# Optimization experiments

Hardware: AMD Instinct MI355X
Metric: run time of the kernel (lower is better)

Reference implementation:

```python
import jax, jax.numpy as jnp
import numpy as np

T, B, EMBED, HEADS = 1024, 32, 512, 8
HEAD = EMBED // HEADS      # per-head value size (= head_dim = 64)
KEYD = 16                  # key_size hard-coded to 16 in MultiheadAttention
MEM_SLOTS, TOPK = 8, 3
NUM_GATES = 2 * EMBED      # gate_style='unit' -> 2*mem_size


def layer_norm(x, g, b, eps=1e-5):
    mu = jnp.mean(x, axis=-1, keepdims=True)
    var = jnp.var(x, axis=-1, keepdims=True)
    return (x - mu) * jax.lax.rsqrt(var + eps) * g + b


def mha(q_src, kv_src, Wq, bq, Wk, bk, Wv, bv, use_topk):
    # q from q_src (RelationalMemory passes 'memory' arg as query source),
    # k/v from kv_src ('input' arg). No 1/sqrt(d) scaling in original code.
    Bq, Sq = q_src.shape[0], q_src.shape[1]
    Sk = kv_src.shape[1]
    q = (q_src @ Wq + bq).reshape(Bq, Sq, HEADS, KEYD)
    k = (kv_src @ Wk + bk).reshape(Bq, Sk, HEADS, KEYD)
    v = (kv_src @ Wv + bv).reshape(Bq, Sk, HEADS, HEAD)
    probs = jax.nn.softmax(jnp.einsum('bqhd,bkhd->bhqk', q, k), axis=-1)
    if use_topk:
        _, idx = jax.lax.top_k(probs, TOPK)  # (B,H,Sq,TOPK)
        mask = jnp.sum(jax.nn.one_hot(idx, Sk, dtype=probs.dtype), axis=-2)
        probs = probs * mask  # post-softmax top-k gate (scatter of ones)
    out = jnp.einsum('bhqk,bkhd->bqhd', probs, v)
    return out.reshape(Bq, Sq, EMBED)


def setup_inputs() -> dict:
    rng = jax.random.key(0)
    ks = jax.random.split(rng, 12)

    def n(k, shape, s=0.02):
        return jax.random.normal(k, shape, dtype=jnp.float32) * s

    # initial_state: eye(mem_slots) zero-padded to mem_size, per batch element
    mem0 = jnp.pad(jnp.eye(MEM_SLOTS, dtype=jnp.float32), ((0, 0), (0, EMBED - MEM_SLOTS)))
    return {
        'query': jax.random.normal(ks[0], (T, B, EMBED), jnp.float32),
        'key': jax.random.normal(ks[1], (T, B, EMBED), jnp.float32),
        'memory': jnp.tile(mem0[None], (B, 1, 1)),
        'W_in': n(ks[2], (EMBED, EMBED)), 'b_in': jnp.zeros((EMBED,), jnp.float32),
        'Wq': n(ks[3], (EMBED, KEYD * HEADS)), 'bq': jnp.zeros((KEYD * HEADS,), jnp.float32),
        'Wk': n(ks[4], (EMBED, KEYD * HEADS)), 'bk': jnp.zeros((KEYD * HEADS,), jnp.float32),
        'Wv': n(ks[5], (EMBED, EMBED)), 'bv': jnp.zeros((EMBED,), jnp.float32),
        'W_mlp': n(ks[6], (EMBED, EMBED)), 'b_mlp': jnp.zeros((EMBED,), jnp.float32),
        'g1': jnp.ones((EMBED,), jnp.float32), 'be1': jnp.zeros((EMBED,), jnp.float32),
        'g2': jnp.ones((EMBED,), jnp.float32), 'be2': jnp.zeros((EMBED,), jnp.float32),
        'w_rep': jax.random.normal(ks[7], (EMBED,), jnp.float32),
        'W_ig': n(ks[8], (EMBED, NUM_GATES)), 'b_ig': jnp.zeros((NUM_GATES,), jnp.float32),
        'W_mg': n(ks[9], (MEM_SLOTS, EMBED, NUM_GATES)), 'b_mg': jnp.zeros((MEM_SLOTS, NUM_GATES), jnp.float32),
        'forget_bias': jnp.asarray(1.0, jnp.float32),
        'input_bias': jnp.asarray(0.0, jnp.float32),
    }


def reference(query, key, memory, W_in, b_in, Wq, bq, Wk, bk, Wv, bv,
              W_mlp, b_mlp, g1, be1, g2, be2, w_rep, W_ig, b_ig,
              W_mg, b_mg, forget_bias, input_bias):
    # query only shape-checked by the torch module; key carries the content
    inputs = jnp.transpose(key, (1, 0, 2))          # (B, T, E)
    x = inputs @ W_in + b_in                        # input_projector
    # attend_over_memory (num_blocks=1): memory slots query the tokens, top-k write
    attended = mha(memory, x, Wq, bq, Wk, bk, Wv, bv, use_topk=True)
    m = layer_norm(memory + attended, g1, be1)
    mlp = jax.nn.relu(m @ W_mlp + b_mlp)            # attention_mlp_layers=1
    new_mem = layer_norm(m + mlp, g2, be2)
    # gating (gate_style='unit')
    gi = jnp.mean(jax.nn.relu(w_rep * x), axis=1) @ W_ig + b_ig      # RepeatLinear -> (B, 2E)
    gm = jnp.einsum('bsm,smn->bsn', jnp.tanh(memory), W_mg) + b_mg   # GroupLinearLayer -> (B, S, 2E)
    in_g, f_g = jnp.split(gi[:, None, :] + gm, 2, axis=-1)
    in_g = jax.nn.sigmoid(in_g + input_bias)
    f_g = jax.nn.sigmoid(f_g + forget_bias)
    new_mem = in_g * jnp.tanh(new_mem) + f_g * memory
    # broadcast read: every token queries the updated memory (no top-k)
    hx = mha(x, new_mem, Wq, bq, Wk, bk, Wv, bv, use_topk=False)     # (B, T, E)
    return jnp.transpose(hx, (1, 0, 2))             # (T, B, E) as in torch forward
```

## Files before the change

### kernel.cpp

```cpp
#include <hip/hip_runtime.h>
#include <stdint.h>

typedef unsigned short u16;
typedef __bf16 bf16x8 __attribute__((ext_vector_type(8)));
typedef float f32x4 __attribute__((ext_vector_type(4)));


__device__ __forceinline__ u16 f2b(float f) {
  union { __bf16 h; u16 u; } v; v.h = (__bf16)f; return v.u;
}
__device__ __forceinline__ float b2f(u16 h) {
  union { uint32_t u; float f; } v; v.u = ((uint32_t)h) << 16; return v.f;
}
__device__ __forceinline__ void gload_lds16(const void* g, void* l) {
  __builtin_amdgcn_global_load_lds(
      (const __attribute__((address_space(1))) unsigned int*)g,
      (__attribute__((address_space(3))) unsigned int*)l, 16, 0, 0);
}

__global__ void k_prep(const float* __restrict__ W_in, u16* __restrict__ WxT,
                       const float* __restrict__ Wv, u16* __restrict__ WvT,
                       const float* __restrict__ mem, float* __restrict__ tm,
                       const float* __restrict__ b_in, float* __restrict__ bfull,
                       const float* __restrict__ Wk, const float* __restrict__ Wq,
                       u16* __restrict__ WkqTr, u16* __restrict__ WinB,
                       const float* __restrict__ W_mlp, u16* __restrict__ WmlpT,
                       const float* __restrict__ key, u16* __restrict__ keyB) {
  int idx = blockIdx.x * 256 + threadIdx.x;
  if (idx < 262144) {
    int k = idx >> 9, n = idx & 511;
    WxT[n * 512 + k] = f2b(W_in[idx]);
  } else if (idx < 524288) {
    int j = idx - 262144;
    int k = j >> 9, n = j & 511;
    WvT[n * 512 + k] = f2b(Wv[j]);
  } else if (idx < 655360) {
    int j = idx - 524288;
    tm[j] = tanhf(mem[j]);
  } else if (idx < 655872) {
    int j = idx - 655360;
    bfull[j] = b_in[j];
  } else if (idx < 786944) {
    int i = idx - 655872;
    int j = i >> 9, n = i & 511;
    WkqTr[i] = f2b(j < 128 ? Wk[n * 128 + j] : Wq[n * 128 + j - 128]);
  } else if (idx < 1049088) {
    int i = idx - 786944;
    WinB[i] = f2b(W_in[i]);
  } else if (idx < 1311232) {
    int i = idx - 1049088;
    int k = i >> 9, n = i & 511;
    WmlpT[n * 512 + k] = f2b(W_mlp[i]);
  } else {
    int i = idx - 1311232;
    int r = i >> 6, e8 = i & 63;
    int b = r >> 10, t = r & 1023;
    const float* src = key + ((size_t)(t * 32 + b) << 9) + e8 * 8;
    float4 lo = *(const float4*)src;
    float4 hi = *(const float4*)(src + 4);
    bf16x8 o;
    o[0] = (__bf16)lo.x; o[1] = (__bf16)lo.y; o[2] = (__bf16)lo.z; o[3] = (__bf16)lo.w;
    o[4] = (__bf16)hi.x; o[5] = (__bf16)hi.y; o[6] = (__bf16)hi.z; o[7] = (__bf16)hi.w;
    *(bf16x8*)(keyB + ((size_t)r << 9) + e8 * 8) = o;
  }
}

__global__ __launch_bounds__(256) void k_wprep2(
    const u16* __restrict__ A, const u16* __restrict__ Bt, u16* __restrict__ WxT,
    const float* __restrict__ b_in, const float* __restrict__ Wk, const float* __restrict__ Wq,
    const float* __restrict__ bk, const float* __restrict__ bq, float* __restrict__ bfull,
    const float* __restrict__ memory, const float* __restrict__ bqf, float* __restrict__ qm)
{
  const int bid = blockIdx.x;
  const int tid = threadIdx.x;
  if (bid < 8) {
    __shared__ u16 As[128 * 32];
    __shared__ u16 Bs[128 * 32];
    const int m0 = (bid & 1) * 128;
    const int n0 = (bid >> 1) * 128;
    const int lane = tid & 63;
    const int wid = tid >> 6;
    const int wm = (wid >> 1) * 64;
    const int wn = (wid & 1) * 64;
    f32x4 acc[4][4];
    #pragma unroll
    for (int i = 0; i < 4; ++i)
      #pragma unroll
      for (int j = 0; j < 4; ++j) acc[i][j] = (f32x4){0.f, 0.f, 0.f, 0.f};
    for (int kt = 0; kt < 16; ++kt) {
      const int k0 = kt << 5;
      __syncthreads();
      #pragma unroll
      for (int c = 0; c < 2; ++c) {
        int o = c * 2048 + tid * 8;
        int row = o >> 5, ck = o & 31;
        gload_lds16(A + (size_t)(m0 + row) * 512 + k0 + ck, As + o);
        gload_lds16(Bt + (size_t)(n0 + row) * 512 + k0 + ck, Bs + o);
      }
      __syncthreads();
      const int r = lane & 15;
      const int kb = (lane >> 4) * 8;
      bf16x8 af[4], bfr[4];
      #pragma unroll
      for (int i = 0; i < 4; ++i) {
        af[i]  = *(const bf16x8*)(As + (wm + i * 16 + r) * 32 + kb);
        bfr[i] = *(const bf16x8*)(Bs + (wn + i * 16 + r) * 32 + kb);
      }
      #pragma unroll
      for (int i = 0; i < 4; ++i)
        #pragma unroll
        for (int j = 0; j < 4; ++j)
          acc[i][j] = __builtin_amdgcn_mfma_f32_16x16x32_bf16(af[i], bfr[j], acc[i][j], 0, 0, 0);
    }
    const int cl = lane & 15;
    const int rl = (lane >> 4) * 4;
    #pragma unroll
    for (int j = 0; j < 4; ++j) {
      const int col = n0 + wn + j * 16 + cl;
      #pragma unroll
      for (int i = 0; i < 4; ++i) {
        #pragma unroll
        for (int rr = 0; rr < 4; ++rr) {
          const int row = m0 + wm + i * 16 + rl + rr;
          WxT[(size_t)(512 + row) * 512 + col] = f2b(acc[i][j][rr]);
        }
      }
    }
  } else if (bid == 8) {
    __shared__ float bs[512];
    const int j = tid;
    bs[tid] = b_in[tid];
    bs[256 + tid] = b_in[256 + tid];
    __syncthreads();
    const float* W = (j < 128) ? (Wk + j) : (Wq + j - 128);
    float a = 0.f;
    #pragma unroll 8
    for (int n = 0; n < 512; ++n)
      a += bs[n] * W[(size_t)n * 128];
    bfull[512 + j] = a + ((j < 128) ? bk[j] : bq[j - 128]);
  } else {
    const int bs_ = bid - 9;
    const int b = bs_ >> 3, s = bs_ & 7;
    const int col = tid & 127, half = tid >> 7;
    __shared__ float mrow[512];
    __shared__ float part[2][128];
    *(float2*)&mrow[tid * 2] = *(const float2*)&memory[(size_t)(b * 8 + s) * 512 + tid * 2];
    __syncthreads();
    float a = 0.f;
    const int e0 = half * 256;
    for (int e = 0; e < 256; ++e)
      a += mrow[e0 + e] * Wq[(size_t)(e0 + e) * 128 + col];
    part[half][col] = a;
    __syncthreads();
    if (tid < 128)
      qm[(size_t)(b * 8 + s) * 128 + tid] = part[0][tid] + part[1][tid] + bqf[tid];
  }
}

__global__ __launch_bounds__(256) void gemm_xkq(
    const u16* __restrict__ keyB, const u16* __restrict__ Bt,
    const float* __restrict__ bias, u16* __restrict__ x, u16* __restrict__ kq)
{
  __shared__ u16 smem[16384];
  u16* As = smem;
  u16* Bs = smem + 8192;
  const int tid = threadIdx.x;
  const int bid = blockIdx.x;
  const int wgid = (bid & 7) * 192 + (bid >> 3);
  const int m0 = (wgid / 6) * 128;
  const int n0 = (wgid % 6) * 128;
  const int lane = tid & 63;
  const int wid = tid >> 6;
  const int wm = (wid >> 1) * 64;
  const int wn = (wid & 1) * 64;

  f32x4 acc[4][4];
  #pragma unroll
  for (int i = 0; i < 4; ++i)
    #pragma unroll
    for (int j = 0; j < 4; ++j) acc[i][j] = (f32x4){0.f, 0.f, 0.f, 0.f};

  for (int kt = 0; kt < 8; ++kt) {
    const int k0 = kt << 6;
    __syncthreads();
    #pragma unroll
    for (int c = 0; c < 4; ++c) {
      const int q = c * 256 + tid;
      const int row = q >> 3;
      const int c8 = q & 7;
      const int lc = c8 ^ (row & 7);
      gload_lds16(keyB + (size_t)(m0 + row) * 512 + k0 + lc * 8, As + q * 8);
      gload_lds16(Bt   + (size_t)(n0 + row) * 512 + k0 + lc * 8, Bs + q * 8);
    }
    __syncthreads();
    const int r = lane & 15;
    const int hi = lane >> 4;
    bf16x8 af[4][2], bfr[4][2];
    #pragma unroll
    for (int i = 0; i < 4; ++i) {
      const int ra = wm + i * 16 + r;
      const int rb = wn + i * 16 + r;
      #pragma unroll
      for (int kk = 0; kk < 2; ++kk) {
        af[i][kk]  = *(const bf16x8*)(As + ra * 64 + (((kk * 4 + hi)) ^ (ra & 7)) * 8);
        bfr[i][kk] = *(const bf16x8*)(Bs + rb * 64 + (((kk * 4 + hi)) ^ (rb & 7)) * 8);
      }
    }
    #pragma unroll
    for (int kk = 0; kk < 2; ++kk)
      #pragma unroll
      for (int i = 0; i < 4; ++i)
        #pragma unroll
        for (int j = 0; j < 4; ++j)
          acc[i][j] = __builtin_amdgcn_mfma_f32_16x16x32_bf16(af[i][kk], bfr[j][kk], acc[i][j], 0, 0, 0);
  }
  __syncthreads();
  u16* Cs = smem;
  const int cl = lane & 15;
  const int rl = (lane >> 4) * 4;
  #pragma unroll
  for (int j = 0; j < 4; ++j) {
    const int lcol = wn + j * 16 + cl;
    const float bsv = bias[n0 + lcol];
    #pragma unroll
    for (int i = 0; i < 4; ++i)
      #pragma unroll
      for (int rr = 0; rr < 4; ++rr)
        Cs[(wm + i * 16 + rl + rr) * 128 + lcol] = f2b(acc[i][j][rr] + bsv);
  }
  __syncthreads();
  #pragma unroll
  for (int c = 0; c < 8; ++c) {
    const int chunk = c * 256 + tid;
    const int row = chunk >> 4, c8 = chunk & 15;
    uint4 v = *(const uint4*)&Cs[row * 128 + c8 * 8];
    if (n0 < 512)
      *(uint4*)(x + (size_t)(m0 + row) * 512 + n0 + c8 * 8) = v;
    else
      *(uint4*)(kq + (size_t)(m0 + row) * 256 + (n0 - 512) + c8 * 8) = v;
  }
}

__global__ __launch_bounds__(256) void k_scores_topk(
    const float* __restrict__ qm, const u16* __restrict__ kq,
    const u16* __restrict__ x, float* __restrict__ p3, u16* __restrict__ XW)
{
  const int b = blockIdx.x, h = blockIdx.y, s = blockIdx.z;
  const int tid = threadIdx.x;
  __shared__ float swv[4];
  __shared__ int   swi[4];
  __shared__ float ssv[4];

  float q[16];
  const float* qp = qm + ((size_t)(b * 8 + s) * 128 + h * 16);
  #pragma unroll
  for (int d = 0; d < 16; ++d) q[d] = qp[d];

  float sc[4];
  #pragma unroll
  for (int j = 0; j < 4; ++j) {
    const int t = j * 256 + tid;
    const u16* kr = kq + ((size_t)(b * 1024 + t)) * 256 + h * 16;
    uint4 v0 = *(const uint4*)kr;
    uint4 v1 = *(const uint4*)(kr + 8);
    const u16* p0 = (const u16*)&v0;
    const u16* p1 = (const u16*)&v1;
    float a = 0.f;
    #pragma unroll
    for (int d = 0; d < 8; ++d) a += q[d] * b2f(p0[d]);
    #pragma unroll
    for (int d = 0; d < 8; ++d) a += q[8 + d] * b2f(p1[d]);
    sc[j] = a;
  }

  int   seli[3];
  float selv[3];
  float ssum = 0.f;
  #pragma unroll
  for (int pass = 0; pass < 3; ++pass) {
    float bv_ = -1e30f; int bi_ = 1 << 30;
    #pragma unroll
    for (int j = 0; j < 4; ++j) {
      const int t = j * 256 + tid;
      bool skip = false;
      for (int k = 0; k < pass; ++k) skip |= (t == seli[k]);
      float v = skip ? -1e30f : sc[j];
      if (v > bv_ || (v == bv_ && t < bi_)) { bv_ = v; bi_ = t; }
    }
    #pragma unroll
    for (int o = 32; o > 0; o >>= 1) {
      float ov = __shfl_xor(bv_, o);
      int   oi = __shfl_xor(bi_, o);
      if (ov > bv_ || (ov == bv_ && oi < bi_)) { bv_ = ov; bi_ = oi; }
    }
    __syncthreads();
    if ((tid & 63) == 0) { swv[tid >> 6] = bv_; swi[tid >> 6] = bi_; }
    __syncthreads();
    float wv = swv[0]; int wi = swi[0];
    #pragma unroll
    for (int w = 1; w < 4; ++w) {
      float ov = swv[w]; int oi = swi[w];
      if (ov > wv || (ov == wv && oi < wi)) { wv = ov; wi = oi; }
    }
    selv[pass] = wv; seli[pass] = wi;

    if (pass == 0) {
      float se = 0.f;
      #pragma unroll
      for (int j = 0; j < 4; ++j) se += __expf(sc[j] - wv);
      #pragma unroll
      for (int o = 32; o > 0; o >>= 1) se += __shfl_xor(se, o);
      __syncthreads();
      if ((tid & 63) == 0) ssv[tid >> 6] = se;
      __syncthreads();
      ssum = ssv[0] + ssv[1] + ssv[2] + ssv[3];
    }
  }

  const float m0v = selv[0];
  const float inv = 1.f / ssum;
  const float p0 = __expf(selv[0] - m0v) * inv;
  const float p1 = __expf(selv[1] - m0v) * inv;
  const float p2 = __expf(selv[2] - m0v) * inv;
  if (tid == 0) {
    const size_t base = (size_t)(b * 64 + h * 8 + s);
    p3[base * 4 + 0] = p0;
    p3[base * 4 + 1] = p1;
    p3[base * 4 + 2] = p2;
    p3[base * 4 + 3] = p0 + p1 + p2;
  }
  if (tid < 64) {
    const u16* xb = x + ((size_t)b << 19) + tid * 8;
    uint4 a0 = *(const uint4*)(xb + ((size_t)seli[0] << 9));
    uint4 a1 = *(const uint4*)(xb + ((size_t)seli[1] << 9));
    uint4 a2 = *(const uint4*)(xb + ((size_t)seli[2] << 9));
    const u16* e0 = (const u16*)&a0;
    const u16* e1 = (const u16*)&a1;
    const u16* e2 = (const u16*)&a2;
    u16 ov[8];
    #pragma unroll
    for (int k = 0; k < 8; ++k)
      ov[k] = f2b(p0 * b2f(e0[k]) + p1 * b2f(e1[k]) + p2 * b2f(e2[k]));
    *(uint4*)(XW + (size_t)h * 131072 + (size_t)(b * 8 + s) * 512 + tid * 8) = *(const uint4*)ov;
  }
}

__global__ __launch_bounds__(256) void k_attgemm(
    const u16* __restrict__ XW, const u16* __restrict__ WvT,
    const float* __restrict__ p3, const float* __restrict__ bvv,
    float* __restrict__ att)
{
  __shared__ u16 As[128 * 32];
  __shared__ u16 Bs[64 * 32];
  const int h = blockIdx.x;
  const int m0 = blockIdx.y * 128;
  const int tid = threadIdx.x;
  const int lane = tid & 63;
  const int wid = tid >> 6;
  const int wm = wid * 32;
  const u16* A = XW + (size_t)h * 131072;
  const u16* Bh = WvT + (size_t)h * 64 * 512;

  f32x4 acc[2][4];
  #pragma unroll
  for (int i = 0; i < 2; ++i)
    #pragma unroll
    for (int j = 0; j < 4; ++j) acc[i][j] = (f32x4){0.f, 0.f, 0.f, 0.f};

  for (int kt = 0; kt < 16; ++kt) {
    const int k0 = kt << 5;
    __syncthreads();
    #pragma unroll
    for (int c = 0; c < 2; ++c) {
      int o = c * 2048 + tid * 8;
      int row = o >> 5, ck = o & 31;
      gload_lds16(A + (size_t)(m0 + row) * 512 + k0 + ck, As + o);
    }
    {
      int row = tid >> 2, ck = (tid & 3) * 8;
      gload_lds16(Bh + (size_t)row * 512 + k0 + ck, Bs + row * 32 + ck);
    }
    __syncthreads();
    const int r = lane & 15;
    const int kb = (lane >> 4) * 8;
    bf16x8 af[2], bfr[4];
    #pragma unroll
    for (int i = 0; i < 2; ++i)
      af[i] = *(const bf16x8*)(As + (wm + i * 16 + r) * 32 + kb);
    #pragma unroll
    for (int j = 0; j < 4; ++j)
      bfr[j] = *(const bf16x8*)(Bs + (j * 16 + r) * 32 + kb);
    #pragma unroll
    for (int i = 0; i < 2; ++i)
      #pragma unroll
      for (int j = 0; j < 4; ++j)
        acc[i][j] = __builtin_amdgcn_mfma_f32_16x16x32_bf16(af[i], bfr[j], acc[i][j], 0, 0, 0);
  }
  const int cl = lane & 15;
  const int rl = (lane >> 4) * 4;
  #pragma unroll
  for (int i = 0; i < 2; ++i) {
    #pragma unroll
    for (int rr = 0; rr < 4; ++rr) {
      const int row = m0 + wm + i * 16 + rl + rr;
      const int bb = row >> 3, ss = row & 7;
      const float sp = p3[(size_t)(bb * 64 + h * 8 + ss) * 4 + 3];
      #pragma unroll
      for (int j = 0; j < 4; ++j) {
        const int col = h * 64 + j * 16 + cl;
        att[(size_t)row * 512 + col] = acc[i][j][rr] + sp * bvv[col];
      }
    }
  }
}

__global__ __launch_bounds__(256) void k_gipre(
    const u16* __restrict__ x, const float* __restrict__ w_rep,
    float* __restrict__ gpart)
{
  const int b = blockIdx.x, ch = blockIdx.y;
  const int tid = threadIdx.x;
  const int e8 = tid & 63, tp = tid >> 6;
  float w[8], acc[8];
  #pragma unroll
  for (int k = 0; k < 8; ++k) { w[k] = w_rep[e8 * 8 + k]; acc[k] = 0.f; }
  const int t0 = ch * 128 + tp * 32;
  for (int tt = 0; tt < 32; ++tt) {
    uint4 v = *(const uint4*)(x + ((size_t)(b * 1024 + t0 + tt) << 9) + e8 * 8);
    const u16* pv = (const u16*)&v;
    #pragma unroll
    for (int k = 0; k < 8; ++k) acc[k] += fmaxf(w[k] * b2f(pv[k]), 0.f);
  }
  __shared__ float ps[4][512];
  #pragma unroll
  for (int k = 0; k < 8; ++k) ps[tp][e8 * 8 + k] = acc[k];
  __syncthreads();
  #pragma unroll
  for (int r = 0; r < 2; ++r) {
    int e = r * 256 + tid;
    gpart[(size_t)(b * 8 + ch) * 512 + e] = ps[0][e] + ps[1][e] + ps[2][e] + ps[3][e];
  }
}

__global__ __launch_bounds__(256) void k_ln1(
    const float* __restrict__ memory, const float* __restrict__ att,
    const float* __restrict__ g1, const float* __restrict__ be1,
    float* __restrict__ m_f32, u16* __restrict__ m_bf)
{
  const int b = blockIdx.x, s = blockIdx.y;
  const int tid = threadIdx.x;
  __shared__ float r1[256], r2[256];
  const size_t base = (size_t)(b * 8 + s) * 512;
  float v0 = memory[base + tid] + att[base + tid];
  float v1 = memory[base + 256 + tid] + att[base + 256 + tid];
  r1[tid] = v0 + v1; r2[tid] = v0 * v0 + v1 * v1;
  __syncthreads();
  for (int off = 128; off > 0; off >>= 1) {
    if (tid < off) { r1[tid] += r1[tid + off]; r2[tid] += r2[tid + off]; }
    __syncthreads();
  }
  float mu = r1[0] * (1.f / 512.f);
  float var = r2[0] * (1.f / 512.f) - mu * mu;
  float rs = rsqrtf(var + 1e-5f);
  float m0v = (v0 - mu) * rs * g1[tid] + be1[tid];
  float m1v = (v1 - mu) * rs * g1[tid + 256] + be1[tid + 256];
  m_f32[base + tid] = m0v;
  m_f32[base + 256 + tid] = m1v;
  m_bf[base + tid] = f2b(m0v);
  m_bf[base + 256 + tid] = f2b(m1v);
}

__global__ __launch_bounds__(256) void gemm_mlp(
    const u16* __restrict__ A, const u16* __restrict__ Bt,
    const float* __restrict__ b_mlp, const float* __restrict__ m_f32,
    float* __restrict__ hbuf)
{
  __shared__ u16 As[128 * 64];
  __shared__ u16 Bs[128 * 64];
  const int tid = threadIdx.x;
  const int m0 = (blockIdx.x >> 2) * 128;
  const int n0 = (blockIdx.x & 3) * 128;
  const int lane = tid & 63;
  const int wid = tid >> 6;
  const int wm = (wid >> 1) * 64;
  const int wn = (wid & 1) * 64;

  f32x4 acc[4][4];
  #pragma unroll
  for (int i = 0; i < 4; ++i)
    #pragma unroll
    for (int j = 0; j < 4; ++j) acc[i][j] = (f32x4){0.f, 0.f, 0.f, 0.f};

  for (int kt = 0; kt < 8; ++kt) {
    const int k0 = kt << 6;
    __syncthreads();
    #pragma unroll
    for (int c = 0; c < 4; ++c) {
      const int q = c * 256 + tid;
      const int row = q >> 3;
      const int c8 = q & 7;
      const int lc = c8 ^ (row & 7);
      gload_lds16(A  + (size_t)(m0 + row) * 512 + k0 + lc * 8, As + q * 8);
      gload_lds16(Bt + (size_t)(n0 + row) * 512 + k0 + lc * 8, Bs + q * 8);
    }
    __syncthreads();
    const int r = lane & 15;
    const int hi = lane >> 4;
    bf16x8 af[4][2], bfr[4][2];
    #pragma unroll
    for (int i = 0; i < 4; ++i) {
      const int ra = wm + i * 16 + r;
      const int rb = wn + i * 16 + r;
      #pragma unroll
      for (int kk = 0; kk < 2; ++kk) {
        af[i][kk]  = *(const bf16x8*)(As + ra * 64 + (((kk * 4 + hi)) ^ (ra & 7)) * 8);
        bfr[i][kk] = *(const bf16x8*)(Bs + rb * 64 + (((kk * 4 + hi)) ^ (rb & 7)) * 8);
      }
    }
    #pragma unroll
    for (int kk = 0; kk < 2; ++kk)
      #pragma unroll
      for (int i = 0; i < 4; ++i)
        #pragma unroll
        for (int j = 0; j < 4; ++j)
          acc[i][j] = __builtin_amdgcn_mfma_f32_16x16x32_bf16(af[i][kk], bfr[j][kk], acc[i][j], 0, 0, 0);
  }
  const int cl = lane & 15;
  const int rl = (lane >> 4) * 4;
  #pragma unroll
  for (int j = 0; j < 4; ++j) {
    const int col = n0 + wn + j * 16 + cl;
    const float bsv = b_mlp[col];
    #pragma unroll
    for (int i = 0; i < 4; ++i) {
      #pragma unroll
      for (int rr = 0; rr < 4; ++rr) {
        const int row = m0 + wm + i * 16 + rl + rr;
        hbuf[(size_t)row * 512 + col] = m_f32[(size_t)row * 512 + col] + fmaxf(acc[i][j][rr] + bsv, 0.f);
      }
    }
  }
}

__global__ __launch_bounds__(256) void k_ln2gate(
    const float* __restrict__ hbuf, const float* __restrict__ g2, const float* __restrict__ be2,
    const float* __restrict__ gip, const float* __restrict__ gmp,
    const float* __restrict__ b_mg, const float* __restrict__ memory,
    const float* __restrict__ fbias, const float* __restrict__ ibias,
    float* __restrict__ nmem)
{
  const int b = blockIdx.x, s = blockIdx.y;
  const int tid = threadIdx.x;
  __shared__ float r1[256], r2[256];
  const size_t base = (size_t)(b * 8 + s) * 512;
  float v0 = hbuf[base + tid];
  float v1 = hbuf[base + 256 + tid];
  r1[tid] = v0 + v1; r2[tid] = v0 * v0 + v1 * v1;
  __syncthreads();
  for (int off = 128; off > 0; off >>= 1) {
    if (tid < off) { r1[tid] += r1[tid + off]; r2[tid] += r2[tid + off]; }
    __syncthreads();
  }
  float mu = r1[0] * (1.f / 512.f);
  float var = r2[0] * (1.f / 512.f) - mu * mu;
  float rs = rsqrtf(var + 1e-5f);
  const float fb = fbias[0], ib = ibias[0];
  #pragma unroll
  for (int rr = 0; rr < 2; ++rr) {
    const int e = rr * 256 + tid;
    const float v = (rr == 0) ? v0 : v1;
    float ln = (v - mu) * rs * g2[e] + be2[e];
    float gin = b_mg[s * 1024 + e], gfn = b_mg[s * 1024 + 512 + e];
    #pragma unroll
    for (int kc = 0; kc < 8; ++kc) {
      size_t gp = (size_t)((kc * 32 + b) * 8 + s) * 1024;
      gin += gmp[gp + e];
      gfn += gmp[gp + 512 + e];
    }
    float giv_i = gip[(size_t)b * 1024 + e]       + gip[(size_t)(32 + b) * 1024 + e];
    float giv_f = gip[(size_t)b * 1024 + 512 + e] + gip[(size_t)(32 + b) * 1024 + 512 + e];
    float ing = 1.f / (1.f + __expf(-(giv_i + gin + ib)));
    float fg  = 1.f / (1.f + __expf(-(giv_f + gfn + fb)));
    nmem[base + e] = ing * tanhf(ln) + fg * memory[base + e];
  }
}

__global__ __launch_bounds__(256) void k_gigm_part(
    const float* __restrict__ tm, const float* __restrict__ W_mg, float* __restrict__ gmp,
    const float* __restrict__ gpart, const float* __restrict__ W_ig,
    const float* __restrict__ b_ig, float* __restrict__ gip)
{
  const int bid = blockIdx.x;
  const int tid = threadIdx.x;
  if (bid < 256) {
    const int s = bid >> 5, nc = (bid >> 3) & 3, kc = bid & 7;
    const int col = nc * 256 + tid;
    const int k0 = kc * 64;
    __shared__ float tms[32][64];
    {
      int i = tid * 2;
      int b = i >> 4, k4 = i & 15;
      *(float4*)&tms[b][k4 * 4] = *(const float4*)&tm[(size_t)(b * 8 + s) * 512 + k0 + k4 * 4];
      i++;
      b = i >> 4; k4 = i & 15;
      *(float4*)&tms[b][k4 * 4] = *(const float4*)&tm[(size_t)(b * 8 + s) * 512 + k0 + k4 * 4];
    }
    __syncthreads();
    float acc[32];
    #pragma unroll
    for (int b = 0; b < 32; ++b) acc[b] = 0.f;
    const float* wp = W_mg + (size_t)s * 524288 + (size_t)k0 * 1024 + col;
    #pragma unroll 2
    for (int kk = 0; kk < 64; ++kk) {
      float w = wp[(size_t)kk << 10];
      #pragma unroll
      for (int b = 0; b < 32; ++b) acc[b] += tms[b][kk] * w;
    }
    #pragma unroll
    for (int b = 0; b < 32; ++b)
      gmp[(size_t)((kc * 32 + b) * 8 + s) * 1024 + col] = acc[b];
  } else {
    const int j = bid - 256;
    const int b = j >> 3, rem = j & 7;
    const int nc = rem >> 1, kc = rem & 1;
    const int k0 = kc * 256;
    const int col = nc * 256 + tid;
    __shared__ float gp[256];
    float a0 = 0.f;
    #pragma unroll
    for (int ch = 0; ch < 8; ++ch) a0 += gpart[(size_t)(b * 8 + ch) * 512 + k0 + tid];
    gp[tid] = a0 * (1.f / 1024.f);
    __syncthreads();
    float a = (kc == 0) ? b_ig[col] : 0.f;
    #pragma unroll 4
    for (int k = 0; k < 256; ++k)
      a += gp[k] * W_ig[(size_t)(k0 + k) * 1024 + col];
    gip[(size_t)(kc * 32 + b) * 1024 + col] = a;
  }
}

__global__ __launch_bounds__(256) void k_kv_part(
    const float* __restrict__ nmem, const float* __restrict__ Wk, const float* __restrict__ Wv,
    float* __restrict__ kvp)
{
  const int b = blockIdx.x, nc = blockIdx.y, kc = blockIdx.z;
  const int tid = threadIdx.x;
  const int col = tid & 127, rg = tid >> 7;
  const int k0 = kc * 128;
  __shared__ float nm[8][128];
  {
    int s = tid >> 5, k4 = tid & 31;
    *(float4*)&nm[s][k4 * 4] = *(const float4*)&nmem[(size_t)(b * 8 + s) * 512 + k0 + k4 * 4];
  }
  __syncthreads();
  const int cg = nc * 128 + col;
  const float* wp; int stride;
  if (nc == 0) { wp = Wk + (size_t)k0 * 128 + cg; stride = 128; }
  else         { wp = Wv + (size_t)k0 * 512 + (cg - 128); stride = 512; }
  const int b0 = rg * 4;
  float a0 = 0.f, a1 = 0.f, a2 = 0.f, a3 = 0.f;
  #pragma unroll 4
  for (int kk = 0; kk < 128; ++kk) {
    float w = wp[(size_t)kk * stride];
    a0 += nm[b0][kk] * w;
    a1 += nm[b0 + 1][kk] * w;
    a2 += nm[b0 + 2][kk] * w;
    a3 += nm[b0 + 3][kk] * w;
  }
  kvp[(size_t)((kc * 32 + b) * 8 + b0    ) * 640 + cg] = a0;
  kvp[(size_t)((kc * 32 + b) * 8 + b0 + 1) * 640 + cg] = a1;
  kvp[(size_t)((kc * 32 + b) * 8 + b0 + 2) * 640 + cg] = a2;
  kvp[(size_t)((kc * 32 + b) * 8 + b0 + 3) * 640 + cg] = a3;
}

__global__ __launch_bounds__(256) void k_out_attn(
    const u16* __restrict__ kq, const float* __restrict__ kvp,
    const float* __restrict__ bk, const float* __restrict__ bv,
    float* __restrict__ out)
{
  int b = blockIdx.x, tc = blockIdx.y;
  int tid = threadIdx.x;
  __shared__ float km[1024];
  __shared__ float vm[4096];
  __shared__ float pr[1024];
  for (int i = tid; i < 1024; i += 256) {
    int s = i >> 7, j = i & 127;
    float a = bk[j];
    #pragma unroll
    for (int kc = 0; kc < 4; ++kc)
      a += kvp[(size_t)((kc * 32 + b) * 8 + s) * 640 + j];
    km[i] = a;
  }
  for (int i = tid; i < 4096; i += 256) {
    int s = i >> 9, c = i & 511;
    float a = bv[c];
    #pragma unroll
    for (int kc = 0; kc < 4; ++kc)
      a += kvp[(size_t)((kc * 32 + b) * 8 + s) * 640 + 128 + c];
    vm[i] = a;
  }
  __syncthreads();
  if (tid < 128) {
    int tt = tid >> 3, hh = tid & 7;
    int t = tc * 16 + tt;
    const u16* qrow = kq + ((size_t)(b * 1024 + t)) * 256 + 128 + hh * 16;
    float q[16];
    #pragma unroll
    for (int d = 0; d < 16; ++d) q[d] = b2f(qrow[d]);
    float s8[8]; float mx = -1e38f;
    #pragma unroll
    for (int s = 0; s < 8; ++s) {
      float a = 0.f;
      #pragma unroll
      for (int d = 0; d < 16; ++d) a += q[d] * km[s * 128 + hh * 16 + d];
      s8[s] = a; mx = fmaxf(mx, a);
    }
    float se = 0.f;
    #pragma unroll
    for (int s = 0; s < 8; ++s) { s8[s] = __expf(s8[s] - mx); se += s8[s]; }
    float inv = 1.f / se;
    #pragma unroll
    for (int s = 0; s < 8; ++s) pr[(tt * 8 + hh) * 8 + s] = s8[s] * inv;
  }
  __syncthreads();
  #pragma unroll
  for (int oi = 0; oi < 8; ++oi) {
    int o = oi * 256 + tid;
    int tt = o >> 7, c4 = o & 127;
    int c = c4 * 4, hh = c >> 6;
    const float* prp = &pr[(tt * 8 + hh) * 8];
    float4 r = {0.f, 0.f, 0.f, 0.f};
    #pragma unroll
    for (int s = 0; s < 8; ++s) {
      float p = prp[s];
      float4 v = *(const float4*)&vm[s * 512 + c];
      r.x += p * v.x; r.y += p * v.y; r.z += p * v.z; r.w += p * v.w;
    }
    int t = tc * 16 + tt;
    *(float4*)&out[((size_t)t * 32 + b) * 512 + c] = r;
  }
}

extern "C" void kernel_launch(void* const* d_in, const int* in_sizes, int n_in,
                              void* d_out, int out_size, void* d_ws, size_t ws_size,
                              hipStream_t stream) {
  (void)in_sizes; (void)n_in; (void)out_size; (void)ws_size;
  const float* key   = (const float*)d_in[1];
  const float* memory= (const float*)d_in[2];
  const float* W_in  = (const float*)d_in[3];
  const float* b_in  = (const float*)d_in[4];
  const float* Wq    = (const float*)d_in[5];
  const float* bq    = (const float*)d_in[6];
  const float* Wk    = (const float*)d_in[7];
  const float* bk    = (const float*)d_in[8];
  const float* Wv    = (const float*)d_in[9];
  const float* bv    = (const float*)d_in[10];
  const float* W_mlp = (const float*)d_in[11];
  const float* b_mlp = (const float*)d_in[12];
  const float* g1    = (const float*)d_in[13];
  const float* be1   = (const float*)d_in[14];
  const float* g2    = (const float*)d_in[15];
  const float* be2   = (const float*)d_in[16];
  const float* w_rep = (const float*)d_in[17];
  const float* W_ig  = (const float*)d_in[18];
  const float* b_ig  = (const float*)d_in[19];
  const float* W_mg  = (const float*)d_in[20];
  const float* b_mg  = (const float*)d_in[21];
  const float* fbias = (const float*)d_in[22];
  const float* ibias = (const float*)d_in[23];
  float* out = (float*)d_out;

  char* p = (char*)d_ws;
  auto alloc = [&](size_t bytes) { char* r = p; p += (bytes + 255) & ~(size_t)255; return r; };
  u16* x       = (u16*)alloc(33554432);
  u16* keyB    = (u16*)alloc(33554432);
  u16* kq      = (u16*)alloc(16777216);
  u16* WxT     = (u16*)alloc(786432);
  u16* WvT     = (u16*)alloc(524288);
  u16* WkqTr   = (u16*)alloc(262144);
  u16* WinB    = (u16*)alloc(524288);
  u16* WmlpT   = (u16*)alloc(524288);
  float* bfull = (float*)alloc(3072);
  float* gpart = (float*)alloc(524288);
  float* gip   = (float*)alloc(262144);
  float* gmp   = (float*)alloc(8388608);
  float* att   = (float*)alloc(524288);
  float* m_f32 = (float*)alloc(524288);
  u16*   m_bf  = (u16*)alloc(262144);
  float* hbuf  = (float*)alloc(524288);
  float* nmem  = (float*)alloc(524288);
  float* kvp   = (float*)alloc(2621440);
  float* tm    = (float*)alloc(524288);
  float* qmw   = (float*)alloc(131072);
  float* p3    = (float*)alloc(32768);
  u16* XW      = (u16*)alloc(2097152);

  k_prep<<<13314, 256, 0, stream>>>(W_in, WxT, Wv, WvT, memory, tm, b_in, bfull,
                                    Wk, Wq, WkqTr, WinB, W_mlp, WmlpT, key, keyB);
  k_wprep2<<<265, 256, 0, stream>>>(WkqTr, WinB, WxT, b_in, Wk, Wq, bk, bq, bfull,
                                    memory, bq, qmw);
  gemm_xkq<<<1536, 256, 0, stream>>>(keyB, WxT, bfull, x, kq);
  k_scores_topk<<<dim3(32, 8, 8), 256, 0, stream>>>(qmw, kq, x, p3, XW);
  k_attgemm<<<dim3(8, 2), 256, 0, stream>>>(XW, WvT, p3, bv, att);
  k_gipre<<<dim3(32, 8), 256, 0, stream>>>(x, w_rep, gpart);
  k_ln1<<<dim3(32, 8), 256, 0, stream>>>(memory, att, g1, be1, m_f32, m_bf);
  gemm_mlp<<<8, 256, 0, stream>>>(m_bf, WmlpT, b_mlp, m_f32, hbuf);
  k_gigm_part<<<512, 256, 0, stream>>>(tm, W_mg, gmp, gpart, W_ig, b_ig, gip);
  k_ln2gate<<<dim3(32, 8), 256, 0, stream>>>(hbuf, g2, be2, gip, gmp, b_mg, memory,
                                             fbias, ibias, nmem);
  k_kv_part<<<dim3(32, 5, 4), 256, 0, stream>>>(nmem, Wk, Wv, kvp);
  k_out_attn<<<dim3(32, 64), 256, 0, stream>>>(kq, kvp, bk, bv, out);
}
```

Before: 196.2 us.

## Stage gate weight tiles in LDS and batch W_ig GEMV across all batches

The W_mg part now fills a 64x256 weight tile in LDS with asynchronous global-to-LDS loads before the FMA loop, instead of issuing strided global loads per k. The W_ig part is restructured from per-batch GEMV blocks (256) into 32 blocks that each handle all 32 batches over a 64-wide K slice. Each W_ig element is then read once rather than once per batch. This splits the input-gate sum into 8 K-partials, so the gip buffer grows and k_ln2gate sums 8 partials instead of 2. Each block uses 72KB of LDS, which limits occupancy.

Result: faster. 187.1 us (-4.6%).

```diff
diff --git a/kernel.cpp b/kernel.cpp
--- a/kernel.cpp
+++ b/kernel.cpp
@@ -577,8 +577,13 @@
       gin += gmp[gp + e];
       gfn += gmp[gp + 512 + e];
     }
-    float giv_i = gip[(size_t)b * 1024 + e]       + gip[(size_t)(32 + b) * 1024 + e];
-    float giv_f = gip[(size_t)b * 1024 + 512 + e] + gip[(size_t)(32 + b) * 1024 + 512 + e];
+    float giv_i = 0.f, giv_f = 0.f;
+    #pragma unroll
+    for (int kc = 0; kc < 8; ++kc) {
+      size_t gp = (size_t)(kc * 32 + b) * 1024;
+      giv_i += gip[gp + e];
+      giv_f += gip[gp + 512 + e];
+    }
     float ing = 1.f / (1.f + __expf(-(giv_i + gin + ib)));
     float fg  = 1.f / (1.f + __expf(-(giv_f + gfn + fb)));
     nmem[base + e] = ing * tanhf(ln) + fg * memory[base + e];
@@ -590,52 +595,76 @@
     const float* __restrict__ gpart, const float* __restrict__ W_ig,
     const float* __restrict__ b_ig, float* __restrict__ gip)
 {
+  __shared__ float wtile[64 * 256];
+  __shared__ float vals[32 * 64];
   const int bid = blockIdx.x;
   const int tid = threadIdx.x;
   if (bid < 256) {
     const int s = bid >> 5, nc = (bid >> 3) & 3, kc = bid & 7;
-    const int col = nc * 256 + tid;
     const int k0 = kc * 64;
-    __shared__ float tms[32][64];
+    const float* wsrc = W_mg + (size_t)s * 524288 + (size_t)k0 * 1024 + nc * 256;
+    #pragma unroll
+    for (int i = 0; i < 16; ++i) {
+      const int q = i * 256 + tid;
+      const int row = q >> 6, c16 = q & 63;
+      gload_lds16(wsrc + (size_t)row * 1024 + c16 * 4, wtile + q * 4);
+    }
     {
       int i = tid * 2;
       int b = i >> 4, k4 = i & 15;
-      *(float4*)&tms[b][k4 * 4] = *(const float4*)&tm[(size_t)(b * 8 + s) * 512 + k0 + k4 * 4];
+      *(float4*)&vals[b * 64 + k4 * 4] = *(const float4*)&tm[(size_t)(b * 8 + s) * 512 + k0 + k4 * 4];
       i++;
       b = i >> 4; k4 = i & 15;
-      *(float4*)&tms[b][k4 * 4] = *(const float4*)&tm[(size_t)(b * 8 + s) * 512 + k0 + k4 * 4];
-    }
-    __syncthreads();
+      *(float4*)&vals[b * 64 + k4 * 4] = *(const float4*)&tm[(size_t)(b * 8 + s) * 512 + k0 + k4 * 4];
+    }
+    __syncthreads();
+    const int col = nc * 256 + tid;
     float acc[32];
     #pragma unroll
     for (int b = 0; b < 32; ++b) acc[b] = 0.f;
-    const float* wp = W_mg + (size_t)s * 524288 + (size_t)k0 * 1024 + col;
-    #pragma unroll 2
     for (int kk = 0; kk < 64; ++kk) {
-      float w = wp[(size_t)kk << 10];
-      #pragma unroll
-      for (int b = 0; b < 32; ++b) acc[b] += tms[b][kk] * w;
+      float w = wtile[kk * 256 + tid];
+      #pragma unroll
+      for (int b = 0; b < 32; ++b) acc[b] += vals[b * 64 + kk] * w;
     }
     #pragma unroll
     for (int b = 0; b < 32; ++b)
       gmp[(size_t)((kc * 32 + b) * 8 + s) * 1024 + col] = acc[b];
   } else {
     const int j = bid - 256;
-    const int b = j >> 3, rem = j & 7;
-    const int nc = rem >> 1, kc = rem & 1;
-    const int k0 = kc * 256;
+    const int nc = j >> 3, kc = j & 7;
+    const int k0 = kc * 64;
+    const float* wsrc = W_ig + (size_t)k0 * 1024 + nc * 256;
+    #pragma unroll
+    for (int i = 0; i < 16; ++i) {
+      const int q = i * 256 + tid;
+      const int row = q >> 6, c16 = q & 63;
+      gload_lds16(wsrc + (size_t)row * 1024 + c16 * 4, wtile + q * 4);
+    }
+    #pragma unroll
+    for (int i = 0; i < 8; ++i) {
+      const int idx = i * 256 + tid;
+      const int b = idx >> 6, k = idx & 63;
+      float a = 0.f;
+      #pragma unroll
+      for (int ch = 0; ch < 8; ++ch)
+        a += gpart[(size_t)(b * 8 + ch) * 512 + k0 + k];
+      vals[b * 64 + k] = a * (1.f / 1024.f);
+    }
+    __syncthreads();
     const int col = nc * 256 + tid;
-    __shared__ float gp[256];
-    float a0 = 0.f;
-    #pragma unroll
-    for (int ch = 0; ch < 8; ++ch) a0 += gpart[(size_t)(b * 8 + ch) * 512 + k0 + tid];
-    gp[tid] = a0 * (1.f / 1024.f);
-    __syncthreads();
-    float a = (kc == 0) ? b_ig[col] : 0.f;
-    #pragma unroll 4
-    for (int k = 0; k < 256; ++k)
-      a += gp[k] * W_ig[(size_t)(k0 + k) * 1024 + col];
-    gip[(size_t)(kc * 32 + b) * 1024 + col] = a;
+    float acc[32];
+    #pragma unroll
+    for (int b = 0; b < 32; ++b) acc[b] = 0.f;
+    for (int kk = 0; kk < 64; ++kk) {
+      float w = wtile[kk * 256 + tid];
+      #pragma unroll
+      for (int b = 0; b < 32; ++b) acc[b] += vals[b * 64 + kk] * w;
+    }
+    const float badd = (kc == 0) ? b_ig[col] : 0.f;
+    #pragma unroll
+    for (int b = 0; b < 32; ++b)
+      gip[(size_t)(kc * 32 + b) * 1024 + col] = acc[b] + badd;
   }
 }
 
@@ -782,7 +811,7 @@
   u16* WmlpT   = (u16*)alloc(524288);
   float* bfull = (float*)alloc(3072);
   float* gpart = (float*)alloc(524288);
-  float* gip   = (float*)alloc(262144);
+  float* gip   = (float*)alloc(1048576);
   float* gmp   = (float*)alloc(8388608);
   float* att   = (float*)alloc(524288);
   float* m_f32 = (float*)alloc(524288);
@@ -805,7 +834,7 @@
   k_gipre<<<dim3(32, 8), 256, 0, stream>>>(x, w_rep, gpart);
   k_ln1<<<dim3(32, 8), 256, 0, stream>>>(memory, att, g1, be1, m_f32, m_bf);
   gemm_mlp<<<8, 256, 0, stream>>>(m_bf, WmlpT, b_mlp, m_f32, hbuf);
-  k_gigm_part<<<512, 256, 0, stream>>>(tm, W_mg, gmp, gpart, W_ig, b_ig, gip);
+  k_gigm_part<<<288, 256, 0, stream>>>(tm, W_mg, gmp, gpart, W_ig, b_ig, gip);
   k_ln2gate<<<dim3(32, 8), 256, 0, stream>>>(hbuf, g2, be2, gip, gmp, b_mg, memory,
                                              fbias, ibias, nmem);
   k_kv_part<<<dim3(32, 5, 4), 256, 0, stream>>>(nmem, Wk, Wv, kvp);
```
